# Kernel tuning notes

Hardware: AMD Instinct MI355X
Metric: run time of the kernel (lower is better)

## Reference

```python
import jax, jax.numpy as jnp
import numpy as np

N = 50000
E = 600000
D = 128


def setup_inputs() -> dict:
    key = jax.random.key(0)
    ks = jax.random.split(key, 10)
    scale = 1.0 / np.sqrt(D)
    inp = {
        "x": jax.random.normal(ks[0], (N, D), dtype=jnp.float32),
        "edge_index": jax.random.randint(ks[1], (2, E), 0, N, dtype=jnp.int64),
        # layer 0: fc + res_fc (residual=True, activation=relu)
        "W1": jax.random.normal(ks[2], (D, D), dtype=jnp.float32) * scale,
        "R1": jax.random.normal(ks[3], (D, D), dtype=jnp.float32) * scale,
        # layer 1
        "W2": jax.random.normal(ks[4], (D, D), dtype=jnp.float32) * scale,
        "R2": jax.random.normal(ks[5], (D, D), dtype=jnp.float32) * scale,
        # layer 2 (last, encoding=False -> no residual/activation)
        "W3": jax.random.normal(ks[6], (D, D), dtype=jnp.float32) * scale,
        # head Linear(out_dim, out_dim) with bias
        "Wh": jax.random.normal(ks[7], (D, D), dtype=jnp.float32) * scale,
        "bh": jnp.zeros((D,), dtype=jnp.float32),
    }
    return inp


def _gcn_stack(x, row, col, norm, W1, R1, W2, R2, W3, Wh, bh):
    n = x.shape[0]

    def conv(x, W, R, act):
        h = x @ W                                   # [N, D]
        msg = h[row] * norm[:, None]                # gather + per-edge scale [E+N, D]
        agg = jax.ops.segment_sum(msg, col, num_segments=n)  # scatter-add [N, D]
        if R is not None:
            agg = agg + x @ R                       # residual
        if act:
            agg = jax.nn.relu(agg)
        return agg

    x = conv(x, W1, R1, True)
    x = conv(x, W2, R2, True)
    x = conv(x, W3, None, False)
    return x @ Wh + bh


def reference(x, edge_index, W1, R1, W2, R2, W3, Wh, bh):
    n = x.shape[0]
    # add self loops (same edge structure for every layer)
    loops = jnp.arange(n, dtype=edge_index.dtype)
    row = jnp.concatenate([edge_index[0], loops])
    col = jnp.concatenate([edge_index[1], loops])
    # symmetric degree normalization: deg computed over col (incl. self loops)
    deg = jax.ops.segment_sum(jnp.ones_like(col, dtype=x.dtype), col, num_segments=n)
    dinv = deg ** -0.5
    norm = dinv[row] * dinv[col]                    # [E+N]
    return _gcn_stack(x, row, col, norm, W1, R1, W2, R2, W3, Wh, bh)
```

## Files before the change

### kernel.cpp

```cpp
#include <hip/hip_runtime.h>
#include <hip/hip_bf16.h>


#define SCAN_CHUNK 1024

typedef _Float16 half8 __attribute__((ext_vector_type(8)));
typedef _Float16 half4 __attribute__((ext_vector_type(4)));
typedef float floatx4 __attribute__((ext_vector_type(4)));

__global__ __launch_bounds__(256) void prep0_kernel(
        int* __restrict__ cnt, int n, int nzb,
        const float* __restrict__ W1, const float* __restrict__ R1,
        const float* __restrict__ W2, const float* __restrict__ R2,
        const float* __restrict__ W3, const float* __restrict__ Wh,
        _Float16* __restrict__ Wt) {
    int b = blockIdx.x;
    int t = threadIdx.x;
    if (b < nzb) {
        int i = b * 256 + t;
        if (i < n) cnt[i] = 0;
        return;
    }
    int b2 = b - nzb;
    if (b2 < 64) {
        __shared__ float tile[32][33];
        int mat = b2 >> 4, tl = b2 & 15;
        const float* W = (mat == 0) ? W1 : (mat == 1) ? R1 : (mat == 2) ? W2 : R2;
        _Float16* T = Wt + (size_t)mat * 16384;
        int tr = (tl >> 2) * 32, tc = (tl & 3) * 32;
        int i = t >> 3, j4 = t & 7;
        float4 v = *(const float4*)&W[(tr + i) * 128 + tc + j4 * 4];
        tile[i][j4 * 4 + 0] = v.x;
        tile[i][j4 * 4 + 1] = v.y;
        tile[i][j4 * 4 + 2] = v.z;
        tile[i][j4 * 4 + 3] = v.w;
        __syncthreads();
        half4 h;
        h.x = (_Float16)tile[j4 * 4 + 0][i];
        h.y = (_Float16)tile[j4 * 4 + 1][i];
        h.z = (_Float16)tile[j4 * 4 + 2][i];
        h.w = (_Float16)tile[j4 * 4 + 3][i];
        *(half4*)&T[(tc + i) * 128 + tr + j4 * 4] = h;
    } else {
        int bb = b2 - 64;
        _Float16* Wtc = Wt + (size_t)4 * 16384;
        int c = bb * 8 + (t >> 5);
        int k0 = (t & 31) * 4;
        float acc0 = 0.f, acc1 = 0.f, acc2 = 0.f, acc3 = 0.f;
        for (int j = 0; j < 128; ++j) {
            float wh = Wh[j * 128 + c];
            acc0 = fmaf(W3[(k0 + 0) * 128 + j], wh, acc0);
            acc1 = fmaf(W3[(k0 + 1) * 128 + j], wh, acc1);
            acc2 = fmaf(W3[(k0 + 2) * 128 + j], wh, acc2);
            acc3 = fmaf(W3[(k0 + 3) * 128 + j], wh, acc3);
        }
        half4 h;
        h.x = (_Float16)acc0; h.y = (_Float16)acc1;
        h.z = (_Float16)acc2; h.w = (_Float16)acc3;
        *(half4*)&Wtc[c * 128 + k0] = h;
    }
}

__global__ void hist_kernel(const int* __restrict__ col, int* __restrict__ cnt, int E) {
    int i = blockIdx.x * blockDim.x + threadIdx.x;
    if (i < E) atomicAdd(&cnt[col[i]], 1);
}

__global__ __launch_bounds__(256) void scan_reduce_kernel(
        const int* __restrict__ cnt, int* __restrict__ bsum, int n) {
    __shared__ int s[256];
    int b = blockIdx.x, t = threadIdx.x;
    int base = b * SCAN_CHUNK + t * 4;
    int v = 0;
    if (base + 3 < n) {
        int4 q = *(const int4*)&cnt[base];
        v = q.x + q.y + q.z + q.w;
    } else {
        for (int i = 0; i < 4; ++i) if (base + i < n) v += cnt[base + i];
    }
    s[t] = v;
    __syncthreads();
    for (int off = 128; off > 0; off >>= 1) {
        if (t < off) s[t] += s[t + off];
        __syncthreads();
    }
    if (t == 0) bsum[b] = s[0];
}

__global__ __launch_bounds__(1024) void scan_bsum_kernel(
        const int* __restrict__ bsum, int* __restrict__ boff, int nb) {
    __shared__ int s[1024];
    int t = threadIdx.x;
    s[t] = (t < nb) ? bsum[t] : 0;
    __syncthreads();
    for (int off = 1; off < 1024; off <<= 1) {
        int add = (t >= off) ? s[t - off] : 0;
        __syncthreads();
        s[t] += add;
        __syncthreads();
    }
    if (t < nb) boff[t] = (t == 0) ? 0 : s[t - 1];
}

__global__ __launch_bounds__(256) void scan_write_kernel(
        const int* __restrict__ cnt, const int* __restrict__ boff,
        int* __restrict__ row_ptr, int* __restrict__ cursor,
        float* __restrict__ dinv, int n, int E) {
    __shared__ int s[256];
    int b = blockIdx.x, t = threadIdx.x;
    int base = b * SCAN_CHUNK + t * 4;
    int v[4];
    int sum = 0;
    for (int i = 0; i < 4; ++i) {
        v[i] = (base + i < n) ? cnt[base + i] : 0;
        sum += v[i];
    }
    s[t] = sum;
    __syncthreads();
    for (int off = 1; off < 256; off <<= 1) {
        int add = (t >= off) ? s[t - off] : 0;
        __syncthreads();
        s[t] += add;
        __syncthreads();
    }
    int prefix = boff[b] + ((t == 0) ? 0 : s[t - 1]);
    for (int i = 0; i < 4; ++i) {
        if (base + i < n) {
            row_ptr[base + i] = prefix;
            cursor[base + i] = prefix;
            dinv[base + i] = rsqrtf((float)(v[i] + 1));
            prefix += v[i];
        }
    }
    if (b == 0 && t == 0) row_ptr[n] = E;
}

__global__ void fill_kernel(const int* __restrict__ row, const int* __restrict__ colv,
                            const float* __restrict__ dinv, int* __restrict__ cursor,
                            unsigned* __restrict__ csr, int E) {
    int i = blockIdx.x * blockDim.x + threadIdx.x;
    if (i < E) {
        int r = row[i], c = colv[i];
        int p = atomicAdd(&cursor[c], 1);
        _Float16 nrm = (_Float16)(dinv[r] * dinv[c]);
        unsigned hn = (unsigned)__builtin_bit_cast(unsigned short, nrm);
        csr[p] = (unsigned)r | (hn << 16);
    }
}

template <int F32IN>
__global__ __launch_bounds__(256) void gemm_dual_kernel(
        const void* __restrict__ Xv, const _Float16* __restrict__ WtA,
        const _Float16* __restrict__ WtB, _Float16* __restrict__ outA,
        _Float16* __restrict__ outB, int n) {
    __shared__ _Float16 Af[64 * 136];
    __shared__ _Float16 Bt[128 * 136];
    int t = threadIdx.x;
    int r0 = blockIdx.x * 64;

    if (F32IN) {
        const float* X = (const float*)Xv;
#pragma unroll
        for (int i = 0; i < 8; ++i) {
            int flat = i * 256 + t;
            int r = flat >> 5, c4 = flat & 31;
            float4 v = make_float4(0.f, 0.f, 0.f, 0.f);
            if (r0 + r < n) v = ((const float4*)X)[(size_t)(r0 + r) * 32 + c4];
            half4 h;
            h.x = (_Float16)v.x; h.y = (_Float16)v.y;
            h.z = (_Float16)v.z; h.w = (_Float16)v.w;
            *(half4*)&Af[r * 136 + c4 * 4] = h;
        }
    } else {
        const _Float16* X = (const _Float16*)Xv;
#pragma unroll
        for (int i = 0; i < 4; ++i) {
            int flat = i * 256 + t;
            int r = flat >> 4, k8 = flat & 15;
            half8 v = {0, 0, 0, 0, 0, 0, 0, 0};
            if (r0 + r < n) v = *(const half8*)&X[(size_t)(r0 + r) * 128 + k8 * 8];
            *(half8*)&Af[r * 136 + k8 * 8] = v;
        }
    }
#pragma unroll
    for (int i = 0; i < 8; ++i) {
        int flat = i * 256 + t;
        int c = flat >> 4, k8 = flat & 15;
        *(half8*)&Bt[c * 136 + k8 * 8] = *(const half8*)&WtA[c * 128 + k8 * 8];
    }
    __syncthreads();

    int lane = t & 63, w = t >> 6;
    int m = lane & 15, q = lane >> 4;
    int rowb = r0 + w * 16 + q * 4;

    half8 a[4];
#pragma unroll
    for (int s = 0; s < 4; ++s)
        a[s] = *(const half8*)&Af[(w * 16 + m) * 136 + s * 32 + q * 8];

    floatx4 acc[8];
#pragma unroll
    for (int nt = 0; nt < 8; ++nt) acc[nt] = (floatx4){0.f, 0.f, 0.f, 0.f};
#pragma unroll
    for (int s = 0; s < 4; ++s)
#pragma unroll
        for (int nt = 0; nt < 8; ++nt) {
            half8 b = *(const half8*)&Bt[(nt * 16 + m) * 136 + s * 32 + q * 8];
            acc[nt] = __builtin_amdgcn_mfma_f32_16x16x32_f16(a[s], b, acc[nt], 0, 0, 0);
        }
    __syncthreads();
#pragma unroll
    for (int i = 0; i < 8; ++i) {
        int flat = i * 256 + t;
        int c = flat >> 4, k8 = flat & 15;
        *(half8*)&Bt[c * 136 + k8 * 8] = *(const half8*)&WtB[c * 128 + k8 * 8];
    }
#pragma unroll
    for (int nt = 0; nt < 8; ++nt) {
        int col = nt * 16 + m;
#pragma unroll
        for (int r = 0; r < 4; ++r) {
            int gr = rowb + r;
            if (gr < n) outA[(size_t)gr * 128 + col] = (_Float16)acc[nt][r];
        }
    }
    __syncthreads();

#pragma unroll
    for (int nt = 0; nt < 8; ++nt) acc[nt] = (floatx4){0.f, 0.f, 0.f, 0.f};
#pragma unroll
    for (int s = 0; s < 4; ++s)
#pragma unroll
        for (int nt = 0; nt < 8; ++nt) {
            half8 b = *(const half8*)&Bt[(nt * 16 + m) * 136 + s * 32 + q * 8];
            acc[nt] = __builtin_amdgcn_mfma_f32_16x16x32_f16(a[s], b, acc[nt], 0, 0, 0);
        }
#pragma unroll
    for (int nt = 0; nt < 8; ++nt) {
        int col = nt * 16 + m;
#pragma unroll
        for (int r = 0; r < 4; ++r) {
            int gr = rowb + r;
            if (gr < n) outB[(size_t)gr * 128 + col] = (_Float16)acc[nt][r];
        }
    }
}

__global__ __launch_bounds__(256) void gemm_h_kernel(
        const _Float16* __restrict__ X, const _Float16* __restrict__ Wt,
        _Float16* __restrict__ out, int n) {
    __shared__ _Float16 Af[64 * 136];
    __shared__ _Float16 Bt[128 * 136];
    int t = threadIdx.x;
    int r0 = blockIdx.x * 64;

#pragma unroll
    for (int i = 0; i < 4; ++i) {
        int flat = i * 256 + t;
        int r = flat >> 4, k8 = flat & 15;
        half8 v = {0, 0, 0, 0, 0, 0, 0, 0};
        if (r0 + r < n) v = *(const half8*)&X[(size_t)(r0 + r) * 128 + k8 * 8];
        *(half8*)&Af[r * 136 + k8 * 8] = v;
    }
#pragma unroll
    for (int i = 0; i < 8; ++i) {
        int flat = i * 256 + t;
        int c = flat >> 4, k8 = flat & 15;
        *(half8*)&Bt[c * 136 + k8 * 8] = *(const half8*)&Wt[c * 128 + k8 * 8];
    }
    __syncthreads();

    int lane = t & 63, w = t >> 6;
    int m = lane & 15, q = lane >> 4;

    floatx4 acc[8];
#pragma unroll
    for (int nt = 0; nt < 8; ++nt) acc[nt] = (floatx4){0.f, 0.f, 0.f, 0.f};

#pragma unroll
    for (int s = 0; s < 4; ++s) {
        half8 a = *(const half8*)&Af[(w * 16 + m) * 136 + s * 32 + q * 8];
#pragma unroll
        for (int nt = 0; nt < 8; ++nt) {
            half8 b = *(const half8*)&Bt[(nt * 16 + m) * 136 + s * 32 + q * 8];
            acc[nt] = __builtin_amdgcn_mfma_f32_16x16x32_f16(a, b, acc[nt], 0, 0, 0);
        }
    }

    int rowb = r0 + w * 16 + q * 4;
#pragma unroll
    for (int nt = 0; nt < 8; ++nt) {
        int col = nt * 16 + m;
#pragma unroll
        for (int r = 0; r < 4; ++r) {
            int gr = rowb + r;
            if (gr < n) out[(size_t)gr * 128 + col] = (_Float16)acc[nt][r];
        }
    }
}

template <int RELU, int FINAL>
__global__ void spmm_kernel(const _Float16* __restrict__ h, const _Float16* __restrict__ xr,
                            const int* __restrict__ row_ptr, const unsigned* __restrict__ csr,
                            const float* __restrict__ dinv, _Float16* __restrict__ outh,
                            float* __restrict__ outf, const float* __restrict__ bias,
                            int n) {
    int gid = blockIdx.x * blockDim.x + threadIdx.x;
    int node = gid >> 4;
    int fl = gid & 15;
    if (node >= n) return;
    const half8* hp8 = (const half8*)h;

    float acc[8];
#pragma unroll
    for (int j = 0; j < 8; ++j) acc[j] = 0.f;

    int e0 = row_ptr[node], e1 = row_ptr[node + 1];
    for (int e = e0; e < e1; e += 8) {
        unsigned d[8];
        float nn[8];
#pragma unroll
        for (int u = 0; u < 8; ++u) {
            int idx = e + u;
            int act = idx < e1;
            d[u] = csr[act ? idx : e];
            nn[u] = act ? (float)__builtin_bit_cast(_Float16, (unsigned short)(d[u] >> 16))
                        : 0.f;
        }
        half8 v[8];
#pragma unroll
        for (int u = 0; u < 8; ++u)
            v[u] = hp8[(size_t)(d[u] & 0xffffu) * 16 + fl];
#pragma unroll
        for (int u = 0; u < 8; ++u)
#pragma unroll
            for (int j = 0; j < 8; ++j)
                acc[j] = fmaf(nn[u], (float)v[u][j], acc[j]);
    }

    float di = dinv[node];
    float w = di * di;
    half8 hv = hp8[(size_t)node * 16 + fl];
#pragma unroll
    for (int j = 0; j < 8; ++j) acc[j] = fmaf(w, (float)hv[j], acc[j]);
    if (!FINAL && xr) {
        half8 r = ((const half8*)xr)[(size_t)node * 16 + fl];
#pragma unroll
        for (int j = 0; j < 8; ++j) acc[j] += (float)r[j];
    }
    if (RELU) {
#pragma unroll
        for (int j = 0; j < 8; ++j) acc[j] = fmaxf(acc[j], 0.f);
    }
    if (FINAL) {
        float4 b0 = *(const float4*)&bias[fl * 8];
        float4 b1 = *(const float4*)&bias[fl * 8 + 4];
        float4 o0 = make_float4(acc[0] + b0.x, acc[1] + b0.y,
                                acc[2] + b0.z, acc[3] + b0.w);
        float4 o1 = make_float4(acc[4] + b1.x, acc[5] + b1.y,
                                acc[6] + b1.z, acc[7] + b1.w);
        ((float4*)outf)[(size_t)node * 32 + fl * 2] = o0;
        ((float4*)outf)[(size_t)node * 32 + fl * 2 + 1] = o1;
    } else {
        half8 o;
#pragma unroll
        for (int j = 0; j < 8; ++j) o[j] = (_Float16)acc[j];
        ((half8*)outh)[(size_t)node * 16 + fl] = o;
    }
}

extern "C" void kernel_launch(void* const* d_in, const int* in_sizes, int n_in,
                              void* d_out, int out_size, void* d_ws, size_t ws_size,
                              hipStream_t stream) {
    const float* x  = (const float*)d_in[0];
    const int*   ei = (const int*)d_in[1];
    const float* W1 = (const float*)d_in[2];
    const float* R1 = (const float*)d_in[3];
    const float* W2 = (const float*)d_in[4];
    const float* R2 = (const float*)d_in[5];
    const float* W3 = (const float*)d_in[6];
    const float* Wh = (const float*)d_in[7];
    const float* bh = (const float*)d_in[8];
    float* out = (float*)d_out;

    int N = in_sizes[0] / 128;
    int E = in_sizes[1] / 2;

    char* p = (char*)d_ws;
    auto alloc = [&](size_t bytes) {
        char* r = p;
        p += (bytes + 255) & ~(size_t)255;
        return r;
    };
    int*      cnt     = (int*)alloc((size_t)N * 4);
    int*      row_ptr = (int*)alloc((size_t)(N + 1) * 4);
    int*      cursor  = (int*)alloc((size_t)N * 4);
    float*    dinv    = (float*)alloc((size_t)N * 4);
    int*      bsum    = (int*)alloc((size_t)1024 * 4);
    int*      boff    = (int*)alloc((size_t)1024 * 4);
    unsigned* csr     = (unsigned*)alloc((size_t)E * 4);
    _Float16* Wt      = (_Float16*)alloc((size_t)5 * 16384 * 2);
    _Float16* B0h     = (_Float16*)alloc((size_t)N * 128 * 2);
    _Float16* B1h     = (_Float16*)alloc((size_t)N * 128 * 2);
    _Float16* B2h     = (_Float16*)alloc((size_t)N * 128 * 2);

    const int* rowi = ei;
    const int* coli = ei + E;

    int nb = (N + SCAN_CHUNK - 1) / SCAN_CHUNK;
    int nzb = (N + 255) / 256;

    prep0_kernel<<<nzb + 80, 256, 0, stream>>>(cnt, N, nzb, W1, R1, W2, R2, W3, Wh, Wt);
    hist_kernel<<<(E + 255) / 256, 256, 0, stream>>>(coli, cnt, E);
    scan_reduce_kernel<<<nb, 256, 0, stream>>>(cnt, bsum, N);
    scan_bsum_kernel<<<1, 1024, 0, stream>>>(bsum, boff, nb);
    scan_write_kernel<<<nb, 256, 0, stream>>>(cnt, boff, row_ptr, cursor, dinv, N, E);
    fill_kernel<<<(E + 255) / 256, 256, 0, stream>>>(rowi, coli, dinv, cursor, csr, E);

    int gb = (N + 63) / 64;
    int sb = ((size_t)N * 16 + 255) / 256;
    _Float16* Wt1 = Wt;
    _Float16* Rt1 = Wt + 16384;
    _Float16* Wt2 = Wt + 2 * 16384;
    _Float16* Rt2 = Wt + 3 * 16384;
    _Float16* Wtc = Wt + 4 * 16384;

    gemm_dual_kernel<1><<<gb, 256, 0, stream>>>(x, Wt1, Rt1, B0h, B1h, N);
    spmm_kernel<1, 0><<<sb, 256, 0, stream>>>(B0h, B1h, row_ptr, csr, dinv,
                                              B1h, nullptr, nullptr, N);
    gemm_dual_kernel<0><<<gb, 256, 0, stream>>>(B1h, Wt2, Rt2, B0h, B2h, N);
    spmm_kernel<1, 0><<<sb, 256, 0, stream>>>(B0h, B2h, row_ptr, csr, dinv,
                                              B2h, nullptr, nullptr, N);
    gemm_h_kernel<<<gb, 256, 0, stream>>>(B2h, Wtc, B0h, N);
    spmm_kernel<0, 1><<<sb, 256, 0, stream>>>(B0h, nullptr, row_ptr, csr, dinv,
                                              nullptr, out, bh, N);
}
```

Before: 294.3 us.

## Fuse graph-build kernels into one persistent kernel with grid barriers

Merges the histogram, the three scan stages and the CSR fill into a single persistent kernel of 256 blocks, separated by software grid barriers built on atomics. This removes four kernel launches and their inter-kernel gaps on the stream. In exchange, each phase now runs on fewer blocks using grid-stride loops, and correctness depends on all 256 blocks being resident at once. The scan of block sums now assumes at most 256 chunks.

After: 465.7 us. 58.2% more time.

```diff
diff --git a/kernel.cpp b/kernel.cpp
--- a/kernel.cpp
+++ b/kernel.cpp
@@ -3,13 +3,32 @@
 
 
 #define SCAN_CHUNK 1024
+#define GB_BLOCKS 256
 
 typedef _Float16 half8 __attribute__((ext_vector_type(8)));
 typedef _Float16 half4 __attribute__((ext_vector_type(4)));
 typedef float floatx4 __attribute__((ext_vector_type(4)));
 
+__device__ __forceinline__ void grid_barrier(int* bar, int* gen, int nblocks) {
+    __threadfence();
+    __syncthreads();
+    if (threadIdx.x == 0) {
+        int g = __hip_atomic_load(gen, __ATOMIC_ACQUIRE, __HIP_MEMORY_SCOPE_AGENT);
+        int prev = __hip_atomic_fetch_add(bar, 1, __ATOMIC_ACQ_REL, __HIP_MEMORY_SCOPE_AGENT);
+        if (prev == nblocks - 1) {
+            __hip_atomic_store(bar, 0, __ATOMIC_RELAXED, __HIP_MEMORY_SCOPE_AGENT);
+            __hip_atomic_fetch_add(gen, 1, __ATOMIC_RELEASE, __HIP_MEMORY_SCOPE_AGENT);
+        } else {
+            while (__hip_atomic_load(gen, __ATOMIC_ACQUIRE, __HIP_MEMORY_SCOPE_AGENT) == g)
+                __builtin_amdgcn_s_sleep(8);
+        }
+        __threadfence();
+    }
+    __syncthreads();
+}
+
 __global__ __launch_bounds__(256) void prep0_kernel(
-        int* __restrict__ cnt, int n, int nzb,
+        int* __restrict__ cnt, int* __restrict__ barstate, int n, int nzb,
         const float* __restrict__ W1, const float* __restrict__ R1,
         const float* __restrict__ W2, const float* __restrict__ R2,
         const float* __restrict__ W3, const float* __restrict__ Wh,
@@ -19,6 +38,7 @@
     if (b < nzb) {
         int i = b * 256 + t;
         if (i < n) cnt[i] = 0;
+        if (b == 0 && t < 4) barstate[t] = 0;
         return;
     }
     int b2 = b - nzb;
@@ -61,86 +81,84 @@
     }
 }
 
-__global__ void hist_kernel(const int* __restrict__ col, int* __restrict__ cnt, int E) {
-    int i = blockIdx.x * blockDim.x + threadIdx.x;
-    if (i < E) atomicAdd(&cnt[col[i]], 1);
-}
-
-__global__ __launch_bounds__(256) void scan_reduce_kernel(
-        const int* __restrict__ cnt, int* __restrict__ bsum, int n) {
+__global__ __launch_bounds__(256) void graph_build_kernel(
+        const int* __restrict__ rowi, const int* __restrict__ coli,
+        int* __restrict__ cnt, int* __restrict__ bsum, int* __restrict__ boff,
+        int* __restrict__ row_ptr, int* __restrict__ cursor,
+        float* __restrict__ dinv, unsigned* __restrict__ csr,
+        int* __restrict__ barstate, int n, int E, int nchunks) {
+    int b = blockIdx.x, t = threadIdx.x;
+    int* bar = barstate;
+    int* gen = barstate + 1;
     __shared__ int s[256];
-    int b = blockIdx.x, t = threadIdx.x;
-    int base = b * SCAN_CHUNK + t * 4;
-    int v = 0;
-    if (base + 3 < n) {
-        int4 q = *(const int4*)&cnt[base];
-        v = q.x + q.y + q.z + q.w;
-    } else {
-        for (int i = 0; i < 4; ++i) if (base + i < n) v += cnt[base + i];
-    }
-    s[t] = v;
-    __syncthreads();
-    for (int off = 128; off > 0; off >>= 1) {
-        if (t < off) s[t] += s[t + off];
+
+    for (int i = b * 256 + t; i < E; i += GB_BLOCKS * 256)
+        atomicAdd(&cnt[coli[i]], 1);
+    grid_barrier(bar, gen, GB_BLOCKS);
+
+    if (b < nchunks) {
+        int base = b * SCAN_CHUNK + t * 4;
+        int v = 0;
+        if (base + 3 < n) {
+            int4 q = *(const int4*)&cnt[base];
+            v = q.x + q.y + q.z + q.w;
+        } else {
+            for (int i = 0; i < 4; ++i) if (base + i < n) v += cnt[base + i];
+        }
+        s[t] = v;
         __syncthreads();
-    }
-    if (t == 0) bsum[b] = s[0];
-}
-
-__global__ __launch_bounds__(1024) void scan_bsum_kernel(
-        const int* __restrict__ bsum, int* __restrict__ boff, int nb) {
-    __shared__ int s[1024];
-    int t = threadIdx.x;
-    s[t] = (t < nb) ? bsum[t] : 0;
-    __syncthreads();
-    for (int off = 1; off < 1024; off <<= 1) {
-        int add = (t >= off) ? s[t - off] : 0;
+        for (int off = 128; off > 0; off >>= 1) {
+            if (t < off) s[t] += s[t + off];
+            __syncthreads();
+        }
+        if (t == 0) bsum[b] = s[0];
+    }
+    grid_barrier(bar, gen, GB_BLOCKS);
+
+    if (b == 0) {
+        s[t] = (t < nchunks) ? bsum[t] : 0;
         __syncthreads();
-        s[t] += add;
+        for (int off = 1; off < 256; off <<= 1) {
+            int add = (t >= off) ? s[t - off] : 0;
+            __syncthreads();
+            s[t] += add;
+            __syncthreads();
+        }
+        if (t < nchunks) boff[t] = (t == 0) ? 0 : s[t - 1];
+    }
+    grid_barrier(bar, gen, GB_BLOCKS);
+
+    if (b < nchunks) {
+        int base = b * SCAN_CHUNK + t * 4;
+        int v[4];
+        int sum = 0;
+        for (int i = 0; i < 4; ++i) {
+            v[i] = (base + i < n) ? cnt[base + i] : 0;
+            sum += v[i];
+        }
+        s[t] = sum;
         __syncthreads();
-    }
-    if (t < nb) boff[t] = (t == 0) ? 0 : s[t - 1];
-}
-
-__global__ __launch_bounds__(256) void scan_write_kernel(
-        const int* __restrict__ cnt, const int* __restrict__ boff,
-        int* __restrict__ row_ptr, int* __restrict__ cursor,
-        float* __restrict__ dinv, int n, int E) {
-    __shared__ int s[256];
-    int b = blockIdx.x, t = threadIdx.x;
-    int base = b * SCAN_CHUNK + t * 4;
-    int v[4];
-    int sum = 0;
-    for (int i = 0; i < 4; ++i) {
-        v[i] = (base + i < n) ? cnt[base + i] : 0;
-        sum += v[i];
-    }
-    s[t] = sum;
-    __syncthreads();
-    for (int off = 1; off < 256; off <<= 1) {
-        int add = (t >= off) ? s[t - off] : 0;
-        __syncthreads();
-        s[t] += add;
-        __syncthreads();
-    }
-    int prefix = boff[b] + ((t == 0) ? 0 : s[t - 1]);
-    for (int i = 0; i < 4; ++i) {
-        if (base + i < n) {
-            row_ptr[base + i] = prefix;
-            cursor[base + i] = prefix;
-            dinv[base + i] = rsqrtf((float)(v[i] + 1));
-            prefix += v[i];
-        }
-    }
-    if (b == 0 && t == 0) row_ptr[n] = E;
-}
-
-__global__ void fill_kernel(const int* __restrict__ row, const int* __restrict__ colv,
-                            const float* __restrict__ dinv, int* __restrict__ cursor,
-                            unsigned* __restrict__ csr, int E) {
-    int i = blockIdx.x * blockDim.x + threadIdx.x;
-    if (i < E) {
-        int r = row[i], c = colv[i];
+        for (int off = 1; off < 256; off <<= 1) {
+            int add = (t >= off) ? s[t - off] : 0;
+            __syncthreads();
+            s[t] += add;
+            __syncthreads();
+        }
+        int prefix = boff[b] + ((t == 0) ? 0 : s[t - 1]);
+        for (int i = 0; i < 4; ++i) {
+            if (base + i < n) {
+                row_ptr[base + i] = prefix;
+                cursor[base + i] = prefix;
+                dinv[base + i] = rsqrtf((float)(v[i] + 1));
+                prefix += v[i];
+            }
+        }
+        if (b == 0 && t == 0) row_ptr[n] = E;
+    }
+    grid_barrier(bar, gen, GB_BLOCKS);
+
+    for (int i = b * 256 + t; i < E; i += GB_BLOCKS * 256) {
+        int r = rowi[i], c = coli[i];
         int p = atomicAdd(&cursor[c], 1);
         _Float16 nrm = (_Float16)(dinv[r] * dinv[c]);
         unsigned hn = (unsigned)__builtin_bit_cast(unsigned short, nrm);
@@ -393,30 +411,30 @@
         p += (bytes + 255) & ~(size_t)255;
         return r;
     };
-    int*      cnt     = (int*)alloc((size_t)N * 4);
-    int*      row_ptr = (int*)alloc((size_t)(N + 1) * 4);
-    int*      cursor  = (int*)alloc((size_t)N * 4);
-    float*    dinv    = (float*)alloc((size_t)N * 4);
-    int*      bsum    = (int*)alloc((size_t)1024 * 4);
-    int*      boff    = (int*)alloc((size_t)1024 * 4);
-    unsigned* csr     = (unsigned*)alloc((size_t)E * 4);
-    _Float16* Wt      = (_Float16*)alloc((size_t)5 * 16384 * 2);
-    _Float16* B0h     = (_Float16*)alloc((size_t)N * 128 * 2);
-    _Float16* B1h     = (_Float16*)alloc((size_t)N * 128 * 2);
-    _Float16* B2h     = (_Float16*)alloc((size_t)N * 128 * 2);
+    int*      cnt      = (int*)alloc((size_t)N * 4);
+    int*      row_ptr  = (int*)alloc((size_t)(N + 1) * 4);
+    int*      cursor   = (int*)alloc((size_t)N * 4);
+    float*    dinv     = (float*)alloc((size_t)N * 4);
+    int*      bsum     = (int*)alloc((size_t)1024 * 4);
+    int*      boff     = (int*)alloc((size_t)1024 * 4);
+    int*      barstate = (int*)alloc((size_t)16 * 4);
+    unsigned* csr      = (unsigned*)alloc((size_t)E * 4);
+    _Float16* Wt       = (_Float16*)alloc((size_t)5 * 16384 * 2);
+    _Float16* B0h      = (_Float16*)alloc((size_t)N * 128 * 2);
+    _Float16* B1h      = (_Float16*)alloc((size_t)N * 128 * 2);
+    _Float16* B2h      = (_Float16*)alloc((size_t)N * 128 * 2);
 
     const int* rowi = ei;
     const int* coli = ei + E;
 
-    int nb = (N + SCAN_CHUNK - 1) / SCAN_CHUNK;
+    int nchunks = (N + SCAN_CHUNK - 1) / SCAN_CHUNK;
     int nzb = (N + 255) / 256;
 
-    prep0_kernel<<<nzb + 80, 256, 0, stream>>>(cnt, N, nzb, W1, R1, W2, R2, W3, Wh, Wt);
-    hist_kernel<<<(E + 255) / 256, 256, 0, stream>>>(coli, cnt, E);
-    scan_reduce_kernel<<<nb, 256, 0, stream>>>(cnt, bsum, N);
-    scan_bsum_kernel<<<1, 1024, 0, stream>>>(bsum, boff, nb);
-    scan_write_kernel<<<nb, 256, 0, stream>>>(cnt, boff, row_ptr, cursor, dinv, N, E);
-    fill_kernel<<<(E + 255) / 256, 256, 0, stream>>>(rowi, coli, dinv, cursor, csr, E);
+    prep0_kernel<<<nzb + 80, 256, 0, stream>>>(cnt, barstate, N, nzb,
+                                               W1, R1, W2, R2, W3, Wh, Wt);
+    graph_build_kernel<<<GB_BLOCKS, 256, 0, stream>>>(
+        rowi, coli, cnt, bsum, boff, row_ptr, cursor, dinv, csr,
+        barstate, N, E, nchunks);
 
     int gb = (N + 63) / 64;
     int sb = ((size_t)N * 16 + 255) / 256;
```
